# Performance work log

Measured on AMD Instinct MI355X. Metric: run time of the kernel, lower is better.

Reference implementation:

```python
import jax, jax.numpy as jnp
import numpy as np

B, S, DIM, HEADS, HD, FF = 2, 2048, 1024, 16, 64, 4096
PREV, MAX_SEQ, THETA, POS_BIAS_MAX, EPS = 1024, 4096, 10000.0, 2.0, 1e-6


def _freqs_cos_sin():
    inv = 1.0 / THETA ** (np.arange(0, HD, 2)[: HD // 2].astype(np.float32) / HD)
    f = np.outer(np.arange(MAX_SEQ, dtype=np.float32), inv)
    return jnp.asarray(np.cos(f), jnp.float32), jnp.asarray(np.sin(f), jnp.float32)


def setup_inputs():
    key = jax.random.key(0)
    ks = jax.random.split(key, 16)
    lin = lambda k, o, i: 0.02 * jax.random.normal(k, (o, i), jnp.float32)
    cos, sin = _freqs_cos_sin()
    return {
        "x": jax.random.normal(ks[0], (B, S, DIM), jnp.float32),
        "cache_k": jax.random.normal(ks[1], (B, HEADS, PREV, HD), jnp.float32),
        "cache_v": jax.random.normal(ks[2], (B, HEADS, PREV, HD), jnp.float32),
        "cos": cos, "sin": sin,
        "attn_norm_w": jnp.ones((DIM,), jnp.float32),
        "ffn_norm_w": jnp.ones((DIM,), jnp.float32),
        "wq": lin(ks[3], DIM, DIM), "bq": jnp.zeros((DIM,), jnp.float32),
        "wk": lin(ks[4], DIM, DIM), "bk": jnp.zeros((DIM,), jnp.float32),
        "wv": lin(ks[5], DIM, DIM), "bv": jnp.zeros((DIM,), jnp.float32),
        "wo": lin(ks[6], DIM, DIM), "bo": jnp.zeros((DIM,), jnp.float32),
        "w_gate": lin(ks[7], FF, DIM), "b_gate": jnp.zeros((FF,), jnp.float32),
        "w_value": lin(ks[8], FF, DIM), "b_value": jnp.zeros((FF,), jnp.float32),
        "w_proj": lin(ks[9], DIM, FF), "b_proj": jnp.zeros((DIM,), jnp.float32),
        "cache_limit": 3072,
    }


def _rmsnorm(h, w):
    return h * jax.lax.rsqrt(jnp.mean(h * h, axis=-1, keepdims=True) + EPS) * w


def _rope(t, cos, sin):
    # t: [B,H,L,HD]; cos/sin: [L, HD//2]; rotate interleaved pairs (complex mult)
    t2 = t.reshape(t.shape[:-1] + (HD // 2, 2))
    x0, x1 = t2[..., 0], t2[..., 1]
    c = cos[None, None]
    s = sin[None, None]
    out = jnp.stack([x0 * c - x1 * s, x0 * s + x1 * c], axis=-1)
    return out.reshape(t.shape)


def _forward(x, cache_k, cache_v, cos, sin, attn_norm_w, ffn_norm_w, wq, bq, wk, bk, wv, bv, wo, bo, w_gate, b_gate, w_value, b_value, w_proj, b_proj, cache_limit):
    b, s, d = x.shape
    h = _rmsnorm(x, attn_norm_w)
    shape4 = lambda t: t.reshape(b, s, HEADS, HD).transpose(0, 2, 1, 3)  # [B,H,S,HD]
    q = shape4(h @ wq.T + bq)
    k_new = shape4(h @ wk.T + bk)
    v_new = shape4(h @ wv.T + bv)
    k_all = jnp.concatenate([cache_k, k_new], axis=2)
    v_all = jnp.concatenate([cache_v, v_new], axis=2)
    if cache_limit > 0:
        k_all = k_all[:, :, -cache_limit:, :]
        v_all = v_all[:, :, -cache_limit:, :]
    total = k_all.shape[2]
    prev = total - s
    # RoPE: q at absolute positions prev..prev+s-1, keys at 0..total-1 (mod cache len)
    pos_q = (jnp.arange(s) + prev) % MAX_SEQ
    pos_k = jnp.arange(total) % MAX_SEQ
    q = _rope(q, cos[pos_q], sin[pos_q])
    k = _rope(k_all, cos[pos_k], sin[pos_k])
    # linear positional bias + causal mask over the new-token block only
    slope = POS_BIAS_MAX / max(total - 1, 1)
    j = jnp.arange(total, dtype=jnp.float32)[None, :]
    i_abs = (prev + jnp.arange(s, dtype=jnp.float32))[:, None]
    bias = slope * (j - i_abs)  # [s, total]
    causal = (jnp.arange(total)[None, :] - prev) > jnp.arange(s)[:, None]
    mask = jnp.where(causal, -jnp.inf, bias)
    scores = jnp.einsum('bhsd,bhtd->bhst', q, k) / jnp.sqrt(jnp.float32(HD)) + mask
    attn = jax.nn.softmax(scores, axis=-1)
    ctx = jnp.einsum('bhst,bhtd->bhsd', attn, v_all)
    ctx = ctx.transpose(0, 2, 1, 3).reshape(b, s, d)
    x = x + ctx @ wo.T + bo
    h2 = _rmsnorm(x, ffn_norm_w)
    gated = jax.nn.silu(h2 @ w_gate.T + b_gate) * (h2 @ w_value.T + b_value)
    return x + gated @ w_proj.T + b_proj


def reference(x, cache_k, cache_v, cos, sin, attn_norm_w, ffn_norm_w, wq, bq, wk, bk, wv, bv, wo, bo, w_gate, b_gate, w_value, b_value, w_proj, b_proj, cache_limit):
    return _forward(x, cache_k, cache_v, cos, sin, attn_norm_w, ffn_norm_w, wq, bq, wk, bk, wv, bv, wo, bo, w_gate, b_gate, w_value, b_value, w_proj, b_proj, cache_limit)
```

## Files before the change

### kernel.cpp

```cpp
#include <hip/hip_runtime.h>
#include <stdint.h>

typedef unsigned short u16;
typedef unsigned int   u32;
typedef __bf16 bf16x8 __attribute__((ext_vector_type(8)));
typedef float  f32x4  __attribute__((ext_vector_type(4)));
typedef u32    u32x4  __attribute__((ext_vector_type(4)));
typedef u32    u32x2  __attribute__((ext_vector_type(2)));

#define B_SZ  2
#define S_LEN 2048
#define NH    16
#define HD    64
#define DIM   1024
#define FF    4096
#define T_LEN 3072
#define PREV  1024
#define MROWS (B_SZ * S_LEN)
#define LOG2E 1.44269504f

#define MFMA16 __builtin_amdgcn_mfma_f32_16x16x32_bf16

__device__ __forceinline__ u16 f2bf(float f) {
  u32 u = __builtin_bit_cast(u32, f);
  u32 r = u + 0x7FFFu + ((u >> 16) & 1u);
  return (u16)(r >> 16);
}
__device__ __forceinline__ float bf2f(u16 h) {
  u32 u = ((u32)h) << 16;
  return __builtin_bit_cast(float, u);
}
__device__ __forceinline__ u32 cvtpk(float lo, float hi) {
  u32 r;
  asm("v_cvt_pk_bf16_f32 %0, %1, %2" : "=v"(r) : "v"(lo), "v"(hi));
  return r;
}

__device__ __forceinline__ void gl_lds16(const void* g, void* l) {
  __builtin_amdgcn_global_load_lds(
      (const __attribute__((address_space(1))) u32*)g,
      (__attribute__((address_space(3))) u32*)l, 16, 0, 0);
}

#define GFENCE() asm volatile("" ::: "memory")
#define BARF()                         \
  do {                                 \
    GFENCE();                          \
    __builtin_amdgcn_s_barrier();      \
    GFENCE();                          \
  } while (0)

__global__ __launch_bounds__(256) void cvt_kernel(const float* __restrict__ src,
                                                  u16* __restrict__ dst, int n4) {
  int i = blockIdx.x * 256 + threadIdx.x;
  const int stride = gridDim.x * 256;
  for (; i < n4; i += stride) {
    f32x4 v = *(const f32x4*)&src[(long)i * 4];
    u32x2 o;
    o[0] = (u32)f2bf(v[0]) | ((u32)f2bf(v[1]) << 16);
    o[1] = (u32)f2bf(v[2]) | ((u32)f2bf(v[3]) << 16);
    *(u32x2*)&dst[(long)i * 4] = o;
  }
}

__global__ __launch_bounds__(256) void cvt_qkv_sw_kernel(const float* __restrict__ wq,
                                                         const float* __restrict__ wk,
                                                         const float* __restrict__ wv,
                                                         u16* __restrict__ dst) {
  int i = blockIdx.x * 256 + threadIdx.x;
  const int stride = gridDim.x * 256;
  for (; i < 3 * 131072; i += stride) {
    const int seg = i >> 17;
    const int loc = i & 131071;
    const float* src = (seg == 0) ? wq : (seg == 1) ? wk : wv;
    int row = loc >> 7;
    int g = loc & 127;
    const float* s = &src[((long)row << 10) + g * 8];
    f32x4 a = *(const f32x4*)s;
    f32x4 b = *(const f32x4*)(s + 4);
    u32x4 o;
    o[0] = (u32)f2bf(a[0]) | ((u32)f2bf(a[1]) << 16);
    o[1] = (u32)f2bf(a[2]) | ((u32)f2bf(a[3]) << 16);
    o[2] = (u32)f2bf(b[0]) | ((u32)f2bf(b[1]) << 16);
    o[3] = (u32)f2bf(b[2]) | ((u32)f2bf(b[3]) << 16);
    const int gp = (g & ~7) | ((g & 7) ^ (row & 7));
    *(u32x4*)&dst[((long)seg << 20) + ((long)row << 10) + gp * 8] = o;
  }
}

__global__ __launch_bounds__(256) void cvt_ilv_sw_kernel(const float* __restrict__ wg,
                                                         const float* __restrict__ wval,
                                                         u16* __restrict__ dst) {
  int i = blockIdx.x * 256 + threadIdx.x;
  const int stride = gridDim.x * 256;
  for (; i < FF * 128; i += stride) {
    int j = i >> 7;
    int g = i & 127;
    const float* sg = &wg[((long)j << 10) + g * 8];
    const float* sv = &wval[((long)j << 10) + g * 8];
    f32x4 a = *(const f32x4*)sg;
    f32x4 b = *(const f32x4*)(sg + 4);
    u32x4 og;
    og[0] = (u32)f2bf(a[0]) | ((u32)f2bf(a[1]) << 16);
    og[1] = (u32)f2bf(a[2]) | ((u32)f2bf(a[3]) << 16);
    og[2] = (u32)f2bf(b[0]) | ((u32)f2bf(b[1]) << 16);
    og[3] = (u32)f2bf(b[2]) | ((u32)f2bf(b[3]) << 16);
    f32x4 c = *(const f32x4*)sv;
    f32x4 d = *(const f32x4*)(sv + 4);
    u32x4 ov;
    ov[0] = (u32)f2bf(c[0]) | ((u32)f2bf(c[1]) << 16);
    ov[1] = (u32)f2bf(c[2]) | ((u32)f2bf(c[3]) << 16);
    ov[2] = (u32)f2bf(d[0]) | ((u32)f2bf(d[1]) << 16);
    ov[3] = (u32)f2bf(d[2]) | ((u32)f2bf(d[3]) << 16);
    const int rg = 2 * j, rv = 2 * j + 1;
    const int gpg = (g & ~7) | ((g & 7) ^ (rg & 7));
    const int gpv = (g & ~7) | ((g & 7) ^ (rv & 7));
    *(u32x4*)&dst[((long)rg << 10) + gpg * 8] = og;
    *(u32x4*)&dst[((long)rv << 10) + gpv * 8] = ov;
  }
}

__global__ __launch_bounds__(256) void bias_pack_kernel(const float* __restrict__ bq,
                                                        const float* __restrict__ bk,
                                                        const float* __restrict__ bv,
                                                        const float* __restrict__ bg,
                                                        const float* __restrict__ bval,
                                                        float* __restrict__ bqkv,
                                                        float* __restrict__ bgv) {
  int i = blockIdx.x * 256 + threadIdx.x;
  if (i < 3 * DIM) {
    float v = (i < DIM) ? bq[i] : (i < 2 * DIM) ? bk[i - DIM] : bv[i - 2 * DIM];
    bqkv[i] = v;
  } else if (i < 3 * DIM + FF) {
    int j = i - 3 * DIM;
    bgv[2 * j] = bg[j];
    bgv[2 * j + 1] = bval[j];
  }
}

__global__ __launch_bounds__(256) void rmsnorm_kernel(const float* __restrict__ x,
                                                      const float* __restrict__ w,
                                                      u16* __restrict__ out) {
  const int row = blockIdx.x;
  const int tid = threadIdx.x;
  const long base = (long)row * DIM + tid * 4;
  f32x4 v = *(const f32x4*)&x[base];
  float ss = v[0] * v[0] + v[1] * v[1] + v[2] * v[2] + v[3] * v[3];
#pragma unroll
  for (int d = 1; d <= 32; d <<= 1) ss += __shfl_xor(ss, d, 64);
  __shared__ float red[4];
  if ((tid & 63) == 0) red[tid >> 6] = ss;
  __syncthreads();
  float tot = red[0] + red[1] + red[2] + red[3];
  const float sc = rsqrtf(tot * (1.f / (float)DIM) + 1e-6f);
  f32x4 wv4 = *(const f32x4*)&w[tid * 4];
  u32x2 o;
  o[0] = (u32)f2bf(v[0] * sc * wv4[0]) | ((u32)f2bf(v[1] * sc * wv4[1]) << 16);
  o[1] = (u32)f2bf(v[2] * sc * wv4[2]) | ((u32)f2bf(v[3] * sc * wv4[3]) << 16);
  const int u = tid >> 1, hf = tid & 1;
  const int up = (u & 0x78) | ((u & 7) ^ (row & 7));
  *(u32x2*)&out[(long)row * DIM + up * 8 + hf * 4] = o;
}

template <int EPI>
__global__ __launch_bounds__(512, 2) void gemm256(const u16* __restrict__ A,
                                                  const u16* __restrict__ Bw,
                                                  const float* __restrict__ bias,
                                                  u16* __restrict__ out_bf,
                                                  int N, int K) {
  __shared__ __align__(16) u16 Ab[2][256 * 64];
  __shared__ __align__(16) u16 Bb[2][256 * 64];
  const int tid = threadIdx.x;
  const int lane = tid & 63;
  const int wid = tid >> 6;
  const int wm = wid >> 2, wn = wid & 3;
  const int l15 = lane & 15, lhi = lane >> 4;
  const int c7 = l15 & 7;
  const int nwg = gridDim.x * gridDim.y;
  const int id = blockIdx.y * gridDim.x + blockIdx.x;
  const int cpx = nwg >> 3;
  const int swz = (id & 7) * cpx + (id >> 3);
  const long m0 = (long)(swz / gridDim.x) * 256;
  const long n0 = (long)(swz % gridDim.x) * 256;
  const int NT = K >> 6;

  const int srow = tid >> 3;
  const int sunit = (tid & 7) * 8;
  const u16* agp = A + (m0 + srow) * K + sunit;
  const u16* bgp = Bw + (n0 + srow) * K + sunit;
  const int ldst = tid * 8;

  auto stageA = [&](int kt, int b) {
    const int k0 = kt << 6;
    u16* d = &Ab[b][0];
#pragma unroll
    for (int c = 0; c < 4; ++c)
      gl_lds16(agp + (long)(c * 64) * K + k0, d + c * 4096 + ldst);
  };
  auto stageB = [&](int kt, int b) {
    const int k0 = kt << 6;
    u16* d = &Bb[b][0];
#pragma unroll
    for (int c = 0; c < 4; ++c)
      gl_lds16(bgp + (long)(c * 64) * K + k0, d + c * 4096 + ldst);
  };

#define READ_A(MH)                                                               \
  _Pragma("unroll") for (int m_ = 0; m_ < 4; ++m_) {                             \
    _Pragma("unroll") for (int ks_ = 0; ks_ < 2; ++ks_) {                        \
      Afr[MH][m_ * 2 + ks_] =                                                    \
          *(const bf16x8*)&Ac[(wm * 128 + (MH)*64 + m_ * 16 + l15) * 64 +        \
                              (((ks_ * 4 + lhi) ^ c7) * 8)];                     \
    }                                                                            \
  }
#define READ_B(NH)                                                               \
  _Pragma("unroll") for (int n_ = 0; n_ < 2; ++n_) {                             \
    _Pragma("unroll") for (int ks_ = 0; ks_ < 2; ++ks_) {                        \
      Bfr[NH][n_ * 2 + ks_] =                                                    \
          *(const bf16x8*)&Bc[(wn * 64 + (NH)*32 + n_ * 16 + l15) * 64 +         \
                              (((ks_ * 4 + lhi) ^ c7) * 8)];                     \
    }                                                                            \
  }
#define QUAD(MH, NH)                                                             \
  do {                                                                           \
    __builtin_amdgcn_s_setprio(1);                                               \
    _Pragma("unroll") for (int m_ = 0; m_ < 4; ++m_) {                           \
      _Pragma("unroll") for (int n_ = 0; n_ < 2; ++n_) {                         \
        acc[(MH)*4 + m_][(NH)*2 + n_] =                                          \
            MFMA16(Afr[MH][m_ * 2], Bfr[NH][n_ * 2],                             \
                   acc[(MH)*4 + m_][(NH)*2 + n_], 0, 0, 0);                      \
        acc[(MH)*4 + m_][(NH)*2 + n_] =                                          \
            MFMA16(Afr[MH][m_ * 2 + 1], Bfr[NH][n_ * 2 + 1],                     \
                   acc[(MH)*4 + m_][(NH)*2 + n_], 0, 0, 0);                      \
      }                                                                          \
    }                                                                            \
    __builtin_amdgcn_s_setprio(0);                                               \
  } while (0)

  f32x4 acc[8][4] = {};

  stageA(0, 0);
  stageB(0, 0);
  stageA(1, 1);
  stageB(1, 1);
  asm volatile("s_waitcnt vmcnt(8)" ::: "memory");
  __builtin_amdgcn_s_barrier();
  GFENCE();

  for (int kt = 0; kt < NT; ++kt) {
    const int b = kt & 1;
    const u16* Ac = &Ab[b][0];
    const u16* Bc = &Bb[b][0];
    bf16x8 Afr[2][8], Bfr[2][4];
    READ_A(0);
    READ_B(0);
    BARF();
    QUAD(0, 0);
    BARF();
    READ_A(1);
    READ_B(1);
    BARF();
    QUAD(0, 1);
    BARF();
    if (kt + 2 < NT) stageA(kt + 2, b);
    BARF();
    QUAD(1, 0);
    BARF();
    if (kt + 2 < NT) stageB(kt + 2, b);
    BARF();
    QUAD(1, 1);
    if (kt + 1 < NT) {
      if (kt + 2 < NT)
        asm volatile("s_waitcnt vmcnt(8)" ::: "memory");
      else
        asm volatile("s_waitcnt vmcnt(0)" ::: "memory");
      __builtin_amdgcn_s_barrier();
      GFENCE();
    }
  }
#undef READ_A
#undef READ_B
#undef QUAD

#pragma unroll
  for (int mi = 0; mi < 8; ++mi) {
    const long row0 = m0 + wm * 128 + mi * 16 + lhi * 4;
#pragma unroll
    for (int ni = 0; ni < 4; ++ni) {
      const long col = n0 + wn * 64 + ni * 16 + l15;
      const float bb = bias[col];
#pragma unroll
      for (int r = 0; r < 4; ++r) {
        float v = acc[mi][ni][r] + bb;
        if (EPI == 2) {
          float other = __shfl_xor(v, 1, 64);
          if (!(l15 & 1)) {
            float s = v / (1.f + __expf(-v)) * other;
            out_bf[(row0 + r) * (N >> 1) + (col >> 1)] = f2bf(s);
          }
        } else {
          out_bf[(row0 + r) * N + col] = f2bf(v);
        }
      }
    }
  }
}

template <int EPI, int NB>
__global__ __launch_bounds__(256) void gemm_bt(const u16* __restrict__ A,
                                               const u16* __restrict__ Bw,
                                               const float* __restrict__ bias,
                                               const float* __restrict__ resid,
                                               u16* __restrict__ out_bf,
                                               float* __restrict__ out_f,
                                               int N, int K) {
  constexpr int BHALF = NB / 64;
  constexpr int NFR = NB / 32;
  constexpr int LPT = 2 + BHALF;
  __shared__ __align__(16) u16 As[3][128 * 32];
  __shared__ __align__(16) u16 Bs[3][NB * 32];
  const int tid = threadIdx.x;
  const int lane = tid & 63;
  const int wv = tid >> 6;
  const int wr = wv >> 1, wc = wv & 1;
  const long m0 = (long)blockIdx.y * 128;
  const long n0 = (long)blockIdx.x * NB;

  const int arow = tid >> 2;
  const int acol = (tid & 3) << 3;
  const u16* ag = A + (m0 + arow) * K + acol;
  const u16* bg = Bw + (n0 + arow) * K + acol;
  const long hK = (long)64 * K;

  f32x4 acc[4][NFR] = {};
  const int l15 = lane & 15;
  const int lhi = lane >> 4;
  const int aoff0 = (wr * 64 + l15) * 32 + lhi * 8;
  const int boff0 = (wc * (NB / 2) + l15) * 32 + lhi * 8;
  const int nk = K >> 5;

  auto stage = [&](int t, int buf) {
    const int k0 = t << 5;
    gl_lds16(ag + k0, &As[buf][tid * 8]);
    gl_lds16(ag + k0 + hK, &As[buf][2048 + tid * 8]);
    gl_lds16(bg + k0, &Bs[buf][tid * 8]);
    if (BHALF == 2) gl_lds16(bg + k0 + hK, &Bs[buf][2048 + tid * 8]);
  };

  stage(0, 0);
  stage(1, 1);
  asm volatile("s_waitcnt vmcnt(%0)" ::"n"(LPT) : "memory");
  __builtin_amdgcn_s_barrier();
  GFENCE();

  for (int t = 0; t < nk; ++t) {
    const int cb = t % 3;
    if (t + 2 < nk) stage(t + 2, (t + 2) % 3);
    bf16x8 af[4], bfr[NFR];
#pragma unroll
    for (int i = 0; i < 4; ++i) af[i] = *(const bf16x8*)&As[cb][aoff0 + i * 16 * 32];
#pragma unroll
    for (int j = 0; j < NFR; ++j) bfr[j] = *(const bf16x8*)&Bs[cb][boff0 + j * 16 * 32];
    __builtin_amdgcn_s_setprio(1);
#pragma unroll
    for (int i = 0; i < 4; ++i)
#pragma unroll
      for (int j = 0; j < NFR; ++j)
        acc[i][j] = MFMA16(af[i], bfr[j], acc[i][j], 0, 0, 0);
    __builtin_amdgcn_s_setprio(0);
    if (t + 2 < nk) {
      asm volatile("s_waitcnt vmcnt(%0)" ::"n"(LPT) : "memory");
      __builtin_amdgcn_s_barrier();
      GFENCE();
    } else if (t + 1 < nk) {
      asm volatile("s_waitcnt vmcnt(0)" ::: "memory");
      __builtin_amdgcn_s_barrier();
      GFENCE();
    }
  }

#pragma unroll
  for (int i = 0; i < 4; ++i) {
    const long row0 = m0 + wr * 64 + i * 16 + lhi * 4;
#pragma unroll
    for (int j = 0; j < NFR; ++j) {
      const long col = n0 + wc * (NB / 2) + j * 16 + l15;
      const float bb = bias[col];
#pragma unroll
      for (int r = 0; r < 4; ++r) {
        const long idx = (row0 + r) * N + col;
        float v = acc[i][j][r] + bb;
        if (EPI == 0) out_bf[idx] = f2bf(v);
        else          out_f[idx] = resid[idx] + v;
      }
    }
  }
}

__global__ __launch_bounds__(256) void rope_all_kernel(const u16* __restrict__ qkv,
                                                       const float* __restrict__ cache_k,
                                                       const float* __restrict__ cache_v,
                                                       const float* __restrict__ cosT,
                                                       const float* __restrict__ sinT,
                                                       u16* __restrict__ Q,
                                                       u16* __restrict__ Kall,
                                                       u16* __restrict__ Vtg) {
  const int blk = blockIdx.x;
  if (blk < 2048) {
    int idx = blk * 256 + threadIdx.x;
    int u = idx & 7;
    int s = (idx >> 3) & (S_LEN - 1);
    int bh = idx >> 14;
    int b = bh >> 4, h = bh & 15;
    int pos = PREV + s;
    const float SC = 0.125f * LOG2E;
    const u16* src = qkv + ((long)(b * S_LEN + s)) * (3 * DIM) + h * HD + u * 8;
    u32x4 d = *(const u32x4*)src;
    f32x4 cv = *(const f32x4*)&cosT[(long)pos * 32 + u * 4];
    f32x4 sv = *(const f32x4*)&sinT[(long)pos * 32 + u * 4];
    u32x4 o;
#pragma unroll
    for (int p = 0; p < 4; ++p) {
      float x0 = bf2f((u16)(d[p] & 0xffff));
      float x1 = bf2f((u16)(d[p] >> 16));
      float y0 = (x0 * cv[p] - x1 * sv[p]) * SC;
      float y1 = (x0 * sv[p] + x1 * cv[p]) * SC;
      o[p] = (u32)f2bf(y0) | ((u32)f2bf(y1) << 16);
    }
    *(u32x4*)&Q[((long)bh * S_LEN + s) * HD + u * 8] = o;
  } else if (blk < 5120) {
    int idx = (blk - 2048) * 256 + threadIdx.x;
    int u = idx & 7;
    int t2 = idx >> 3;
    int j = t2 % T_LEN;
    int bh = t2 / T_LEN;
    int b = bh >> 4, h = bh & 15;
    float e[8];
    if (j < PREV) {
      const float* src = cache_k + ((long)bh * PREV + j) * HD + u * 8;
      f32x4 a = *(const f32x4*)src;
      f32x4 c = *(const f32x4*)(src + 4);
      e[0] = a[0]; e[1] = a[1]; e[2] = a[2]; e[3] = a[3];
      e[4] = c[0]; e[5] = c[1]; e[6] = c[2]; e[7] = c[3];
    } else {
      const u16* src = qkv + ((long)(b * S_LEN + (j - PREV))) * (3 * DIM) + DIM + h * HD + u * 8;
      u32x4 d = *(const u32x4*)src;
#pragma unroll
      for (int p = 0; p < 4; ++p) {
        e[2 * p] = bf2f((u16)(d[p] & 0xffff));
        e[2 * p + 1] = bf2f((u16)(d[p] >> 16));
      }
    }
    f32x4 cv = *(const f32x4*)&cosT[(long)j * 32 + u * 4];
    f32x4 sv = *(const f32x4*)&sinT[(long)j * 32 + u * 4];
    u32x4 o;
#pragma unroll
    for (int p = 0; p < 4; ++p) {
      float y0 = e[2 * p] * cv[p] - e[2 * p + 1] * sv[p];
      float y1 = e[2 * p] * sv[p] + e[2 * p + 1] * cv[p];
      o[p] = (u32)f2bf(y0) | ((u32)f2bf(y1) << 16);
    }
    *(u32x4*)&Kall[((long)bh * T_LEN + j) * HD + (u ^ (j & 7)) * 8] = o;
  } else {
    int idx = (blk - 5120) * 256 + threadIdx.x;
    int hd = idx & 63;
    int t2 = idx >> 6;
    int kb = t2 % 384;
    int bh = t2 / 384;
    int b = bh >> 4, h = bh & 15;
    int key0 = kb * 8;
    u16 vals[8];
    if (key0 < PREV) {
#pragma unroll
      for (int i = 0; i < 8; ++i)
        vals[i] = f2bf(cache_v[((long)bh * PREV + key0 + i) * HD + hd]);
    } else {
#pragma unroll
      for (int i = 0; i < 8; ++i)
        vals[i] = qkv[((long)(b * S_LEN + key0 + i - PREV)) * (3 * DIM) + 2 * DIM + h * HD + hd];
    }
    u32x4 o;
#pragma unroll
    for (int p = 0; p < 4; ++p)
      o[p] = (u32)vals[2 * p] | ((u32)vals[2 * p + 1] << 16);
    const int span = kb >> 3;
    const int u = (kb & 7) ^ (hd & 7);
    *(u32x4*)&Vtg[((long)bh * HD + hd) * T_LEN + span * 64 + u * 8] = o;
  }
}

__global__ __launch_bounds__(256, 2) void attn_kernel(const u16* __restrict__ Q,
                                                      const u16* __restrict__ Kg,
                                                      const u16* __restrict__ Vtg,
                                                      u16* __restrict__ ctx, float slope2) {
  __shared__ __align__(16) u16 Ks[2][64 * 64];
  __shared__ __align__(16) u16 Vs[2][64 * 64];
  __shared__ __align__(16) u16 Ps[2][4][16 * 64];

  const int tid = threadIdx.x;
  const int lane = tid & 63;
  const int wv = tid >> 6;
  const int l15 = lane & 15;
  const int lhi = lane >> 4;
  const int c7 = l15 & 7;
  const int bh = blockIdx.x;
  const int p = blockIdx.y;
  const int b = bh >> 4, h = bh & 15;
  const int qA0 = p * 64;
  const int qB0 = (31 - p) * 64;
  const int ntA = 17 + p;
  const int ntB = 48 - p;

  const long qrowA = (long)bh * S_LEN + qA0 + wv * 16 + l15;
  const long qrowB = (long)bh * S_LEN + qB0 + wv * 16 + l15;
  bf16x8 aqA0 = *(const bf16x8*)&Q[qrowA * HD + lhi * 8];
  bf16x8 aqA1 = *(const bf16x8*)&Q[qrowA * HD + 32 + lhi * 8];
  bf16x8 aqB0 = *(const bf16x8*)&Q[qrowB * HD + lhi * 8];
  bf16x8 aqB1 = *(const bf16x8*)&Q[qrowB * HD + 32 + lhi * 8];

  const long kgb = (long)bh * T_LEN * HD;
  const long vgb = (long)bh * HD * T_LEN;
  const int srow = tid >> 3;
  const int sunit = (tid & 7) * 8;

  const u16* kst = Kg + kgb + (long)srow * HD + sunit;
  const u16* vst = Vtg + vgb + (long)srow * T_LEN + sunit;

  gl_lds16(kst, &Ks[0][tid * 8]);
  gl_lds16(kst + 32 * HD, &Ks[0][2048 + tid * 8]);
  gl_lds16(vst, &Vs[0][tid * 8]);
  gl_lds16(vst + (long)32 * T_LEN, &Vs[0][2048 + tid * 8]);
  kst += 64 * HD;
  vst += 64;
  __syncthreads();

  f32x4 oA[4] = {}, oB[4] = {};
  f32x4 lrunA = {0.f, 0.f, 0.f, 0.f}, lrunB = {0.f, 0.f, 0.f, 0.f};
  float mrunA = -1e30f, mrunB = -1e30f;
  const int qq = wv * 16 + l15;

  f32x4 be[4];
#pragma unroll
  for (int jf = 0; jf < 4; ++jf)
#pragma unroll
    for (int r = 0; r < 4; ++r)
      be[jf][r] = slope2 * (float)(jf * 16 + 4 * lhi + r);
  const float bmax = slope2 * 63.f;

  bf16x8 vones;
#pragma unroll
  for (int e = 0; e < 8; ++e) vones[e] = (__bf16)1.0f;

  float ktf = 0.f;
  const float kstep = slope2 * 64.f;

  auto process = [&](f32x4 (&sf)[4], bool maskNow, f32x4 (&o)[4], f32x4& lrun,
                     float& mrun, bf16x8 (&vf)[8], u16* Pw) {
    if (maskNow) {
#pragma unroll
      for (int jf = 0; jf < 4; ++jf)
#pragma unroll
        for (int r = 0; r < 4; ++r)
          if (jf * 16 + 4 * lhi + r > qq) sf[jf][r] = -1e30f;
    }
    float h0 = fmaxf(fmaxf(sf[0][0], sf[0][1]), fmaxf(sf[0][2], sf[0][3]));
    float h1 = fmaxf(fmaxf(sf[1][0], sf[1][1]), fmaxf(sf[1][2], sf[1][3]));
    float h2 = fmaxf(fmaxf(sf[2][0], sf[2][1]), fmaxf(sf[2][2], sf[2][3]));
    float h3 = fmaxf(fmaxf(sf[3][0], sf[3][1]), fmaxf(sf[3][2], sf[3][3]));
    float pm = fmaxf(fmaxf(h0, h1), fmaxf(h2, h3));
    pm = fmaxf(pm, __shfl_xor(pm, 16, 64));
    pm = fmaxf(pm, __shfl_xor(pm, 32, 64));
    const float pmax_abs = pm + ktf + bmax;

    if (!__all(pmax_abs - mrun <= 8.f)) {
      const float mnew = fmaxf(mrun, pmax_abs);
      const float scl = exp2f(mrun - mnew);
      mrun = mnew;
#pragma unroll
      for (int r = 0; r < 4; ++r) {
        const float sr = __shfl(scl, 4 * lhi + r, 64);
        lrun[r] *= sr;
#pragma unroll
        for (int hf = 0; hf < 4; ++hf) o[hf][r] *= sr;
      }
    }
    const float meff = mrun - ktf;

#pragma unroll
    for (int jf = 0; jf < 4; ++jf) {
      f32x4 pp;
#pragma unroll
      for (int r = 0; r < 4; ++r)
        pp[r] = exp2f(sf[jf][r] + (be[jf][r] - meff));
      u32x2 pw2;
      pw2[0] = cvtpk(pp[0], pp[1]);
      pw2[1] = cvtpk(pp[2], pp[3]);
      const int u = (2 * jf + (lhi >> 1)) ^ c7;
      *(u32x2*)&Pw[l15 * 64 + u * 8 + (lhi & 1) * 4] = pw2;
    }

    bf16x8 pa0 = *(const bf16x8*)&Pw[l15 * 64 + ((lhi ^ c7) * 8)];
    bf16x8 pa1 = *(const bf16x8*)&Pw[l15 * 64 + (((4 + lhi) ^ c7) * 8)];
    f32x4 psum = {};
    __builtin_amdgcn_s_setprio(1);
    psum = MFMA16(pa0, vones, psum, 0, 0, 0);
    psum = MFMA16(pa1, vones, psum, 0, 0, 0);
#pragma unroll
    for (int hf = 0; hf < 4; ++hf) {
      o[hf] = MFMA16(pa0, vf[2 * hf], o[hf], 0, 0, 0);
      o[hf] = MFMA16(pa1, vf[2 * hf + 1], o[hf], 0, 0, 0);
    }
    __builtin_amdgcn_s_setprio(0);
    lrun += psum;
  };

  for (int t = 0; t < ntB; ++t) {
    const int cur = t & 1, nxt = cur ^ 1;
    const bool lastStage = (t + 1 == ntB);
    if (!lastStage) {
      gl_lds16(kst, &Ks[nxt][tid * 8]);
      gl_lds16(kst + 32 * HD, &Ks[nxt][2048 + tid * 8]);
      gl_lds16(vst, &Vs[nxt][tid * 8]);
      gl_lds16(vst + (long)32 * T_LEN, &Vs[nxt][2048 + tid * 8]);
      kst += 64 * HD;
      vst += 64;
    }
    const bool actA = (t < ntA);

    bf16x8 kf[8];
#pragma unroll
    for (int jf = 0; jf < 4; ++jf) {
      const int krow = jf * 16 + l15;
      kf[2 * jf] = *(const bf16x8*)&Ks[cur][krow * 64 + ((lhi ^ c7) * 8)];
      kf[2 * jf + 1] = *(const bf16x8*)&Ks[cur][krow * 64 + (((4 + lhi) ^ c7) * 8)];
    }
    bf16x8 vf[8];
#pragma unroll
    for (int hf = 0; hf < 4; ++hf) {
      const int vrow = hf * 16 + l15;
      vf[2 * hf] = *(const bf16x8*)&Vs[cur][vrow * 64 + ((lhi ^ c7) * 8)];
      vf[2 * hf + 1] = *(const bf16x8*)&Vs[cur][vrow * 64 + (((4 + lhi) ^ c7) * 8)];
    }

    f32x4 sB[4], sA[4];
    __builtin_amdgcn_s_setprio(1);
#pragma unroll
    for (int jf = 0; jf < 4; ++jf) {
      f32x4 s = {};
      s = MFMA16(kf[2 * jf], aqB0, s, 0, 0, 0);
      s = MFMA16(kf[2 * jf + 1], aqB1, s, 0, 0, 0);
      sB[jf] = s;
    }
    __builtin_amdgcn_s_setprio(0);
    if (actA) {
      __builtin_amdgcn_s_setprio(1);
#pragma unroll
      for (int jf = 0; jf < 4; ++jf) {
        f32x4 s = {};
        s = MFMA16(kf[2 * jf], aqA0, s, 0, 0, 0);
        s = MFMA16(kf[2 * jf + 1], aqA1, s, 0, 0, 0);
        sA[jf] = s;
      }
      __builtin_amdgcn_s_setprio(0);
    }

    process(sB, t == ntB - 1, oB, lrunB, mrunB, vf, &Ps[0][wv][0]);
    if (actA) process(sA, t == ntA - 1, oA, lrunA, mrunA, vf, &Ps[1][wv][0]);

    ktf += kstep;
    if (!lastStage) __syncthreads();
  }

#pragma unroll
  for (int r = 0; r < 4; ++r) {
    const float invA = 1.f / lrunA[r];
    const float invB = 1.f / lrunB[r];
    const long rowA = (long)b * S_LEN + qA0 + wv * 16 + 4 * lhi + r;
    const long rowB = (long)b * S_LEN + qB0 + wv * 16 + 4 * lhi + r;
#pragma unroll
    for (int hf = 0; hf < 4; ++hf) {
      ctx[rowA * DIM + h * HD + hf * 16 + l15] = f2bf(oA[hf][r] * invA);
      ctx[rowB * DIM + h * HD + hf * 16 + l15] = f2bf(oB[hf][r] * invB);
    }
  }
}

extern "C" void kernel_launch(void* const* d_in, const int* in_sizes, int n_in,
                              void* d_out, int out_size, void* d_ws, size_t ws_size,
                              hipStream_t stream) {
  (void)in_sizes; (void)n_in; (void)out_size; (void)ws_size;
  const float* x       = (const float*)d_in[0];
  const float* cache_k = (const float*)d_in[1];
  const float* cache_v = (const float*)d_in[2];
  const float* cosT    = (const float*)d_in[3];
  const float* sinT    = (const float*)d_in[4];
  const float* attn_w  = (const float*)d_in[5];
  const float* ffn_w   = (const float*)d_in[6];
  const float* wq      = (const float*)d_in[7];
  const float* bq      = (const float*)d_in[8];
  const float* wk      = (const float*)d_in[9];
  const float* bk      = (const float*)d_in[10];
  const float* wv_     = (const float*)d_in[11];
  const float* bv      = (const float*)d_in[12];
  const float* wo      = (const float*)d_in[13];
  const float* bo      = (const float*)d_in[14];
  const float* wg      = (const float*)d_in[15];
  const float* bg      = (const float*)d_in[16];
  const float* wval    = (const float*)d_in[17];
  const float* bval    = (const float*)d_in[18];
  const float* wp      = (const float*)d_in[19];
  const float* bp      = (const float*)d_in[20];
  float* out = (float*)d_out;

  char* w = (char*)d_ws;
  size_t off = 0;
  auto alloc = [&](size_t bytes) -> char* {
    char* p = w + off;
    off += (bytes + 255) & ~(size_t)255;
    return p;
  };
  u16*   wqkv_bf  = (u16*)alloc((size_t)3 * DIM * DIM * 2);
  u16*   wo_bf    = (u16*)alloc((size_t)DIM * DIM * 2);
  u16*   wgv_bf   = (u16*)alloc((size_t)2 * FF * DIM * 2);
  u16*   wproj_bf = (u16*)alloc((size_t)DIM * FF * 2);
  float* bqkv     = (float*)alloc((size_t)3 * DIM * 4);
  float* bgv      = (float*)alloc((size_t)2 * FF * 4);
  float* x2       = (float*)alloc((size_t)MROWS * DIM * 4);
  char* AR = alloc((size_t)117440512);
  u16* qkv   = (u16*)(AR + 0);
  u16* Qb    = (u16*)(AR + 25165824);
  u16* Kb    = (u16*)(AR + 33554432);
  u16* Vtg   = (u16*)(AR + 46137344);
  u16* h1    = (u16*)(AR + 58720256);
  u16* ctx   = (u16*)(AR + 0);
  u16* h2    = (u16*)(AR + 8388608);
  u16* gated = (u16*)(AR + 16777216);

  cvt_qkv_sw_kernel<<<1024, 256, 0, stream>>>(wq, wk, wv_, wqkv_bf);
  cvt_kernel<<<512, 256, 0, stream>>>(wo, wo_bf, DIM * DIM / 4);
  cvt_ilv_sw_kernel<<<1024, 256, 0, stream>>>(wg, wval, wgv_bf);
  cvt_kernel<<<1024, 256, 0, stream>>>(wp, wproj_bf, DIM * FF / 4);
  bias_pack_kernel<<<28, 256, 0, stream>>>(bq, bk, bv, bg, bval, bqkv, bgv);

  rmsnorm_kernel<<<MROWS, 256, 0, stream>>>(x, attn_w, h1);
  gemm256<0><<<dim3(12, 16), 512, 0, stream>>>(h1, wqkv_bf, bqkv, qkv, 3 * DIM, DIM);
  rope_all_kernel<<<8192, 256, 0, stream>>>(qkv, cache_k, cache_v, cosT, sinT,
                                            Qb, Kb, Vtg);
  attn_kernel<<<dim3(B_SZ * NH, 16), 256, 0, stream>>>(
      Qb, Kb, Vtg, ctx, (2.0f / (float)(T_LEN - 1)) * LOG2E);
  gemm_bt<1, 64><<<dim3(16, 32), 256, 0, stream>>>(ctx, wo_bf, bo, x, nullptr, x2,
                                                   DIM, DIM);
  rmsnorm_kernel<<<MROWS, 256, 0, stream>>>(x2, ffn_w, h2);
  gemm256<2><<<dim3(32, 16), 512, 0, stream>>>(h2, wgv_bf, bgv, gated, 2 * FF, DIM);
  gemm_bt<1, 64><<<dim3(16, 32), 256, 0, stream>>>(gated, wproj_bf, bp, x2, nullptr, out,
                                                   DIM, FF);
}
```

Before: 361.1 us.

## Merge weight-conversion kernels, drop tile swizzle, and cut barriers in gemm256 loop

```diff
diff --git a/kernel.cpp b/kernel.cpp
--- a/kernel.cpp
+++ b/kernel.cpp
@@ -50,26 +50,19 @@
     GFENCE();                          \
   } while (0)
 
-__global__ __launch_bounds__(256) void cvt_kernel(const float* __restrict__ src,
-                                                  u16* __restrict__ dst, int n4) {
-  int i = blockIdx.x * 256 + threadIdx.x;
-  const int stride = gridDim.x * 256;
-  for (; i < n4; i += stride) {
-    f32x4 v = *(const f32x4*)&src[(long)i * 4];
-    u32x2 o;
-    o[0] = (u32)f2bf(v[0]) | ((u32)f2bf(v[1]) << 16);
-    o[1] = (u32)f2bf(v[2]) | ((u32)f2bf(v[3]) << 16);
-    *(u32x2*)&dst[(long)i * 4] = o;
-  }
-}
-
-__global__ __launch_bounds__(256) void cvt_qkv_sw_kernel(const float* __restrict__ wq,
-                                                         const float* __restrict__ wk,
-                                                         const float* __restrict__ wv,
-                                                         u16* __restrict__ dst) {
-  int i = blockIdx.x * 256 + threadIdx.x;
-  const int stride = gridDim.x * 256;
-  for (; i < 3 * 131072; i += stride) {
+__global__ __launch_bounds__(256) void cvt_all_kernel(
+    const float* __restrict__ wq, const float* __restrict__ wk,
+    const float* __restrict__ wv, const float* __restrict__ wg,
+    const float* __restrict__ wval, const float* __restrict__ wo,
+    const float* __restrict__ wp, const float* __restrict__ bq,
+    const float* __restrict__ bk, const float* __restrict__ bv,
+    const float* __restrict__ bg, const float* __restrict__ bval,
+    u16* __restrict__ wqkv_bf, u16* __restrict__ wgv_bf,
+    u16* __restrict__ wo_bf, u16* __restrict__ wp_bf,
+    float* __restrict__ bqkv, float* __restrict__ bgv) {
+  long gid = (long)blockIdx.x * 256 + threadIdx.x;
+  if (gid < 393216) {
+    int i = (int)gid;
     const int seg = i >> 17;
     const int loc = i & 131071;
     const float* src = (seg == 0) ? wq : (seg == 1) ? wk : wv;
@@ -84,16 +77,12 @@
     o[2] = (u32)f2bf(b[0]) | ((u32)f2bf(b[1]) << 16);
     o[3] = (u32)f2bf(b[2]) | ((u32)f2bf(b[3]) << 16);
     const int gp = (g & ~7) | ((g & 7) ^ (row & 7));
-    *(u32x4*)&dst[((long)seg << 20) + ((long)row << 10) + gp * 8] = o;
-  }
-}
-
-__global__ __launch_bounds__(256) void cvt_ilv_sw_kernel(const float* __restrict__ wg,
-                                                         const float* __restrict__ wval,
-                                                         u16* __restrict__ dst) {
-  int i = blockIdx.x * 256 + threadIdx.x;
-  const int stride = gridDim.x * 256;
-  for (; i < FF * 128; i += stride) {
+    *(u32x4*)&wqkv_bf[((long)seg << 20) + ((long)row << 10) + gp * 8] = o;
+    return;
+  }
+  gid -= 393216;
+  if (gid < 524288) {
+    int i = (int)gid;
     int j = i >> 7;
     int g = i & 127;
     const float* sg = &wg[((long)j << 10) + g * 8];
@@ -115,26 +104,47 @@
     const int rg = 2 * j, rv = 2 * j + 1;
     const int gpg = (g & ~7) | ((g & 7) ^ (rg & 7));
     const int gpv = (g & ~7) | ((g & 7) ^ (rv & 7));
-    *(u32x4*)&dst[((long)rg << 10) + gpg * 8] = og;
-    *(u32x4*)&dst[((long)rv << 10) + gpv * 8] = ov;
-  }
-}
-
-__global__ __launch_bounds__(256) void bias_pack_kernel(const float* __restrict__ bq,
-                                                        const float* __restrict__ bk,
-                                                        const float* __restrict__ bv,
-                                                        const float* __restrict__ bg,
-                                                        const float* __restrict__ bval,
-                                                        float* __restrict__ bqkv,
-                                                        float* __restrict__ bgv) {
-  int i = blockIdx.x * 256 + threadIdx.x;
-  if (i < 3 * DIM) {
-    float v = (i < DIM) ? bq[i] : (i < 2 * DIM) ? bk[i - DIM] : bv[i - 2 * DIM];
-    bqkv[i] = v;
-  } else if (i < 3 * DIM + FF) {
-    int j = i - 3 * DIM;
-    bgv[2 * j] = bg[j];
-    bgv[2 * j + 1] = bval[j];
+    *(u32x4*)&wgv_bf[((long)rg << 10) + gpg * 8] = og;
+    *(u32x4*)&wgv_bf[((long)rv << 10) + gpv * 8] = ov;
+    return;
+  }
+  gid -= 524288;
+  if (gid < 131072) {
+    int i = (int)gid;
+    f32x4 a = *(const f32x4*)&wo[(long)i * 8];
+    f32x4 b = *(const f32x4*)&wo[(long)i * 8 + 4];
+    u32x4 o;
+    o[0] = (u32)f2bf(a[0]) | ((u32)f2bf(a[1]) << 16);
+    o[1] = (u32)f2bf(a[2]) | ((u32)f2bf(a[3]) << 16);
+    o[2] = (u32)f2bf(b[0]) | ((u32)f2bf(b[1]) << 16);
+    o[3] = (u32)f2bf(b[2]) | ((u32)f2bf(b[3]) << 16);
+    *(u32x4*)&wo_bf[(long)i * 8] = o;
+    return;
+  }
+  gid -= 131072;
+  if (gid < 524288) {
+    int i = (int)gid;
+    f32x4 a = *(const f32x4*)&wp[(long)i * 8];
+    f32x4 b = *(const f32x4*)&wp[(long)i * 8 + 4];
+    u32x4 o;
+    o[0] = (u32)f2bf(a[0]) | ((u32)f2bf(a[1]) << 16);
+    o[1] = (u32)f2bf(a[2]) | ((u32)f2bf(a[3]) << 16);
+    o[2] = (u32)f2bf(b[0]) | ((u32)f2bf(b[1]) << 16);
+    o[3] = (u32)f2bf(b[2]) | ((u32)f2bf(b[3]) << 16);
+    *(u32x4*)&wp_bf[(long)i * 8] = o;
+    return;
+  }
+  gid -= 524288;
+  {
+    int i = (int)gid;
+    if (i < 3 * DIM) {
+      float v = (i < DIM) ? bq[i] : (i < 2 * DIM) ? bk[i - DIM] : bv[i - 2 * DIM];
+      bqkv[i] = v;
+    } else if (i < 3 * DIM + FF) {
+      int j = i - 3 * DIM;
+      bgv[2 * j] = bg[j];
+      bgv[2 * j + 1] = bval[j];
+    }
   }
 }
 
@@ -176,12 +186,8 @@
   const int wm = wid >> 2, wn = wid & 3;
   const int l15 = lane & 15, lhi = lane >> 4;
   const int c7 = l15 & 7;
-  const int nwg = gridDim.x * gridDim.y;
-  const int id = blockIdx.y * gridDim.x + blockIdx.x;
-  const int cpx = nwg >> 3;
-  const int swz = (id & 7) * cpx + (id >> 3);
-  const long m0 = (long)(swz / gridDim.x) * 256;
-  const long n0 = (long)(swz % gridDim.x) * 256;
+  const long m0 = (long)blockIdx.y * 256;
+  const long n0 = (long)blockIdx.x * 256;
   const int NT = K >> 6;
 
   const int srow = tid >> 3;
@@ -254,20 +260,19 @@
     bf16x8 Afr[2][8], Bfr[2][4];
     READ_A(0);
     READ_B(0);
-    BARF();
-    QUAD(0, 0);
-    BARF();
     READ_A(1);
     READ_B(1);
-    BARF();
+    QUAD(0, 0);
+    QUAD(1, 0);
+    asm volatile("s_waitcnt lgkmcnt(0)" ::: "memory");
+    __builtin_amdgcn_sched_barrier(0);
+    __builtin_amdgcn_s_barrier();
+    GFENCE();
+    if (kt + 2 < NT) {
+      stageA(kt + 2, b);
+      stageB(kt + 2, b);
+    }
     QUAD(0, 1);
-    BARF();
-    if (kt + 2 < NT) stageA(kt + 2, b);
-    BARF();
-    QUAD(1, 0);
-    BARF();
-    if (kt + 2 < NT) stageB(kt + 2, b);
-    BARF();
     QUAD(1, 1);
     if (kt + 1 < NT) {
       if (kt + 2 < NT)
@@ -736,11 +741,10 @@
   u16* h2    = (u16*)(AR + 8388608);
   u16* gated = (u16*)(AR + 16777216);
 
-  cvt_qkv_sw_kernel<<<1024, 256, 0, stream>>>(wq, wk, wv_, wqkv_bf);
-  cvt_kernel<<<512, 256, 0, stream>>>(wo, wo_bf, DIM * DIM / 4);
-  cvt_ilv_sw_kernel<<<1024, 256, 0, stream>>>(wg, wval, wgv_bf);
-  cvt_kernel<<<1024, 256, 0, stream>>>(wp, wproj_bf, DIM * FF / 4);
-  bias_pack_kernel<<<28, 256, 0, stream>>>(bq, bk, bv, bg, bval, bqkv, bgv);
+  cvt_all_kernel<<<6172, 256, 0, stream>>>(wq, wk, wv_, wg, wval, wo, wp,
+                                           bq, bk, bv, bg, bval,
+                                           wqkv_bf, wgv_bf, wo_bf, wproj_bf,
+                                           bqkv, bgv);
 
   rmsnorm_kernel<<<MROWS, 256, 0, stream>>>(x, attn_w, h1);
   gemm256<0><<<dim3(12, 16), 512, 0, stream>>>(h1, wqkv_bf, bqkv, qkv, 3 * DIM, DIM);
```

After: 349.2 us (median of 2 runs). -3.3%, faster.
